# Kernel optimization log

Measured on AMD Instinct MI355X. Metric: run time of the kernel, lower is better.

Reference implementation:

```python
import jax, jax.numpy as jnp
import numpy as np

N_NODES = 100000
N_EDGES = 1600000
IN_DIM = 128
HID = 128
OUT_DIM = 64
N_LAYERS = 3


def setup_inputs() -> dict:
    key = jax.random.key(0)
    ks = jax.random.split(key, 8)
    x = jax.random.normal(ks[0], (N_NODES, IN_DIM), dtype=jnp.float32)
    edge_index = jax.random.randint(ks[1], (2, N_EDGES), 0, N_NODES, dtype=jnp.int64)
    s = 1.0 / np.sqrt(HID)
    Wl = jax.random.normal(ks[2], (N_LAYERS, HID, HID), dtype=jnp.float32) * s
    Wr = jax.random.normal(ks[3], (N_LAYERS, HID, HID), dtype=jnp.float32) * s
    b = jnp.zeros((N_LAYERS, HID), dtype=jnp.float32)
    fc_w = jax.random.normal(ks[4], (N_LAYERS * HID, OUT_DIM), dtype=jnp.float32) * (1.0 / np.sqrt(N_LAYERS * HID))
    fc_b = jnp.zeros((OUT_DIM,), dtype=jnp.float32)
    return {"x": x, "edge_index": edge_index, "Wl": Wl, "Wr": Wr, "b": b, "fc_w": fc_w, "fc_b": fc_b}


def _sage_conv(x, src, dst, Wl, Wr, b, n_nodes):
    # PyG SAGEConv (aggr='mean'): out = lin_l(mean_{j->i} x_j) + lin_r(x_i)
    msg = x[src]                                             # [E, d] gather
    agg = jax.ops.segment_sum(msg, dst, num_segments=n_nodes)  # [N, d]
    deg = jax.ops.segment_sum(jnp.ones((src.shape[0],), x.dtype), dst, num_segments=n_nodes)
    mean = agg / jnp.maximum(deg, 1.0)[:, None]
    return mean @ Wl + x @ Wr + b


def reference(x, edge_index, Wl, Wr, b, fc_w, fc_b):
    src, dst = edge_index[0], edge_index[1]
    n = x.shape[0]
    h = x
    layer_out = []
    for i in range(N_LAYERS):  # small fixed layer count
        h = jax.nn.relu(_sage_conv(h, src, dst, Wl[i], Wr[i], b[i], n))
        layer_out.append(h)  # dropout p=0 -> identity
    hk = jnp.concatenate(layer_out, axis=-1)  # JK 'cat': [N, L*HID]
    return hk @ fc_w + fc_b
```

## Files before the change

kernel.cpp:

```cpp
#include <hip/hip_runtime.h>
#include <hip/hip_bf16.h>
#include <stdint.h>

#define N_NODES 100000
#define N_EDGES 1600000
#define HID 128
#define OUT_DIM 64
#define N_LAYERS 3
#define CAP 64
#define CAP_SHIFT 6
#define BIN_NODES 256
#define NBIN2 ((N_NODES + BIN_NODES - 1) / BIN_NODES)
#define BINCAP 8192
#define EPT 8

typedef __attribute__((ext_vector_type(8))) short short8;
typedef __attribute__((ext_vector_type(4))) float v4f;
typedef __attribute__((ext_vector_type(4))) unsigned short ushort4v;

__device__ __forceinline__ float bf2f(unsigned int lo16) {
    union { unsigned int i; float f; } v; v.i = lo16 << 16; return v.f;
}
__device__ __forceinline__ unsigned short f2bf(float f) {
    union { float f; unsigned int i; } v; v.f = f;
    unsigned int r = v.i + 0x7fffu + ((v.i >> 16) & 1u);
    return (unsigned short)(r >> 16);
}

__device__ __forceinline__ void stage16(const void* g, void* l) {
    __builtin_amdgcn_global_load_lds(
        (const __attribute__((address_space(1))) unsigned int*)g,
        (__attribute__((address_space(3))) unsigned int*)l, 16, 0, 0);
}

#define CONV_N (N_NODES * HID / 4)
__global__ void prologue(const int* __restrict__ raw, int* __restrict__ flag,
                         int* __restrict__ bin_cnt,
                         const float* __restrict__ x, unsigned short* __restrict__ xb,
                         const float* __restrict__ Wl, const float* __restrict__ Wr,
                         const float* __restrict__ fc_w,
                         unsigned short* __restrict__ WlT, unsigned short* __restrict__ WrT,
                         unsigned short* __restrict__ fcT,
                         unsigned short* b0, unsigned short* b1, unsigned short* b2) {
    int gidx = blockIdx.x * blockDim.x + threadIdx.x;
    if (blockIdx.x == 0 && threadIdx.x < 64) {
        int v = raw[2 * threadIdx.x + 1];
        unsigned long long b = __ballot(v != 0);
        if (threadIdx.x == 0) *flag = (b == 0ull) ? 1 : 0;
    }
    if (gidx < NBIN2) bin_cnt[gidx] = 0;
    if (blockIdx.x == 1 && threadIdx.x < 192) {
        int t = threadIdx.x;
        unsigned short* bufs[3] = {b0, b1, b2};
        uint32_t* p = (uint32_t*)bufs[t >> 6];
        p[(size_t)N_NODES * 64 + (t & 63)] = 0;
    }

    if (gidx < CONV_N) {
        float4 v = ((const float4*)x)[gidx];
        ushort4v o;
        o[0] = f2bf(v.x); o[1] = f2bf(v.y); o[2] = f2bf(v.z); o[3] = f2bf(v.w);
        ((ushort4v*)xb)[gidx] = o;
        return;
    }
    int idx = gidx - CONV_N;
    const int WELEMS = N_LAYERS * HID * HID;
    if (idx < WELEMS) {
        int l = idx / (HID * HID);
        int rem = idx - l * HID * HID;
        int k = rem / HID, nn2 = rem - k * HID;
        WlT[l * HID * HID + nn2 * HID + k] = f2bf(Wl[idx]);
        WrT[l * HID * HID + nn2 * HID + k] = f2bf(Wr[idx]);
    } else {
        int j = idx - WELEMS;
        if (j < N_LAYERS * HID * OUT_DIM) {
            int l = j / (HID * OUT_DIM);
            int rem = j - l * HID * OUT_DIM;
            int k = rem / OUT_DIM, o = rem - k * OUT_DIM;
            fcT[l * OUT_DIM * HID + o * HID + k] = f2bf(fc_w[(l * HID + k) * OUT_DIM + o]);
        }
    }
}

__global__ __launch_bounds__(256) void fill_p1(const int* __restrict__ raw,
                                               const int* __restrict__ flag,
                                               int* __restrict__ bin_cnt,
                                               unsigned int* __restrict__ bins) {
    __shared__ int h[NBIN2];
    __shared__ int basekeep[NBIN2];
    int tid = threadIdx.x;
    for (int b = tid; b < NBIN2; b += 256) h[b] = 0;
    __syncthreads();

    int e0 = blockIdx.x * (256 * EPT) + tid;
    int s[EPT], d[EPT];
    bool is64 = (*flag != 0);
#pragma unroll
    for (int k = 0; k < EPT; ++k) {
        int e = e0 + k * 256;
        if (e < N_EDGES) {
            if (is64) {
                const long long* r = (const long long*)raw;
                d[k] = (int)r[N_EDGES + e];
                s[k] = (int)r[e];
            } else {
                d[k] = raw[N_EDGES + e];
                s[k] = raw[e];
            }
        } else {
            d[k] = -1;
        }
    }
#pragma unroll
    for (int k = 0; k < EPT; ++k)
        if (d[k] >= 0) atomicAdd(&h[d[k] >> 8], 1);
    __syncthreads();
    for (int b = tid; b < NBIN2; b += 256) {
        int c = h[b];
        basekeep[b] = c ? atomicAdd(&bin_cnt[b], c) : 0;
        h[b] = 0;
    }
    __syncthreads();
#pragma unroll
    for (int k = 0; k < EPT; ++k) {
        if (d[k] >= 0) {
            int b = d[k] >> 8;
            int off = basekeep[b] + atomicAdd(&h[b], 1);
            if (off < BINCAP)
                bins[(size_t)b * BINCAP + off] =
                    ((unsigned int)s[k] << 8) | (unsigned int)(d[k] & 255);
        }
    }
}

__global__ __launch_bounds__(256) void fill_p2(const int* __restrict__ bin_cnt,
                                               const unsigned int* __restrict__ bins,
                                               int* __restrict__ ell,
                                               int* __restrict__ deg,
                                               float* __restrict__ inv_deg, int n) {
    __shared__ int tile[BIN_NODES * CAP];
    __shared__ int cnt[BIN_NODES];
    int b = blockIdx.x, tid = threadIdx.x;
    for (int i = tid; i < BIN_NODES; i += 256) cnt[i] = 0;
    __syncthreads();

    int m = bin_cnt[b];
    if (m > BINCAP) m = BINCAP;
    for (int i = tid; i < m; i += 256) {
        unsigned int e = bins[(size_t)b * BINCAP + i];
        int dl = (int)(e & 255u);
        int slot = atomicAdd(&cnt[dl], 1);
        if (slot < CAP) tile[(dl << CAP_SHIFT) + slot] = (int)(e >> 8);
    }
    __syncthreads();

    int node0 = b << 8;
    for (int i = tid; i < BIN_NODES; i += 256) {
        int node = node0 + i;
        if (node < n) {
            int dgf = cnt[i];
            int dg = dgf > CAP ? CAP : dgf;
            deg[node] = dg;
            inv_deg[node] = 1.0f / (float)(dg > 0 ? dg : 1);
            int r = (dg + 7) & ~7;
            for (int p = dg; p < r; ++p) tile[(i << CAP_SHIFT) + p] = N_NODES;
        }
    }
    __syncthreads();

    const uint4* t4 = (const uint4*)tile;
    uint4* g4 = (uint4*)ell;
    for (int v = tid; v < BIN_NODES * 16; v += 256) {
        int row = v >> 4;
        int node = node0 + row;
        if (node < n) g4[((size_t)node << 4) + (v & 15)] = t4[v];
    }
}

__global__ __launch_bounds__(256) void agg_bf(
    const unsigned short* __restrict__ h, const int* __restrict__ ell,
    const int* __restrict__ deg, const float* __restrict__ inv_deg,
    unsigned short* __restrict__ meanb) {
    int tid = threadIdx.x;
    int grp = tid >> 4;
    int lane16 = tid & 15;
    int node = blockIdx.x * 16 + grp;
    bool valid = node < N_NODES;
    int nd = valid ? node : 0;
    int dg = valid ? deg[nd] : 0;
    int dgp = (dg + 7) & ~7;
    int base = nd << CAP_SHIFT;
    const uint4* hv = (const uint4*)h;
    float a[8];
#pragma unroll
    for (int c = 0; c < 8; ++c) a[c] = 0.f;

    for (int t = 0; t < dgp; t += 8) {
        int idx[8];
#pragma unroll
        for (int u = 0; u < 8; ++u) idx[u] = ell[base + t + u];
        uint4 v[8];
#pragma unroll
        for (int u = 0; u < 8; ++u) v[u] = hv[(size_t)idx[u] * 16 + lane16];
#pragma unroll
        for (int u = 0; u < 8; ++u) {
            a[0] += bf2f(v[u].x & 0xffffu); a[1] += bf2f(v[u].x >> 16);
            a[2] += bf2f(v[u].y & 0xffffu); a[3] += bf2f(v[u].y >> 16);
            a[4] += bf2f(v[u].z & 0xffffu); a[5] += bf2f(v[u].z >> 16);
            a[6] += bf2f(v[u].w & 0xffffu); a[7] += bf2f(v[u].w >> 16);
        }
    }
    if (valid) {
        float id = inv_deg[nd];
        uint4 o;
        o.x = (uint32_t)f2bf(a[0] * id) | ((uint32_t)f2bf(a[1] * id) << 16);
        o.y = (uint32_t)f2bf(a[2] * id) | ((uint32_t)f2bf(a[3] * id) << 16);
        o.z = (uint32_t)f2bf(a[4] * id) | ((uint32_t)f2bf(a[5] * id) << 16);
        o.w = (uint32_t)f2bf(a[6] * id) | ((uint32_t)f2bf(a[7] * id) << 16);
        *(uint4*)&meanb[(size_t)node * HID + lane16 * 8] = o;
    }
}

__global__ __launch_bounds__(256, 2) void layer_mfma(
    const unsigned short* __restrict__ Am,
    const unsigned short* __restrict__ Ah,
    const unsigned short* __restrict__ WlT,
    const unsigned short* __restrict__ WrT,
    const float* __restrict__ bias,
    unsigned short* __restrict__ Hout, int n) {
    __shared__ uint4 smA[128 * 16];
    __shared__ uint4 smB[128 * 16];
    int tid = threadIdx.x;
    int w = tid >> 6, L = tid & 63;
    int q = L >> 4, r16 = L & 15;
    int colbase = (w & 1) * 64;
    int nodebase = (w >> 1) * 64;
    int node0 = blockIdx.x * 128;

    {
        const unsigned short* srcs[2] = {Am, Ah};
#pragma unroll
        for (int op = 0; op < 2; ++op) {
            const unsigned short* S = srcs[op];
            char* D = (char*)(op ? smB : smA);
#pragma unroll
            for (int i = 0; i < 8; ++i) {
                int c = (w << 3) + i;
                int row_l = (c << 2) + (L >> 4);
                int chunk = (L & 15) ^ (row_l & 7);
                const unsigned short* src =
                    S + (((size_t)(node0 + row_l)) << 7) + (chunk << 3);
                stage16(src, D + (c << 10));
            }
        }
    }

    short8 wfr[2][4][4];
#pragma unroll
    for (int seg = 0; seg < 2; ++seg) {
        const unsigned short* WT = seg ? WrT : WlT;
#pragma unroll
        for (int t = 0; t < 4; ++t)
#pragma unroll
            for (int i = 0; i < 4; ++i)
                wfr[seg][t][i] =
                    *(const short8*)&WT[(colbase + i * 16 + r16) * HID + t * 32 + q * 8];
    }

    __syncthreads();

    v4f acc[4][4];
#pragma unroll
    for (int i = 0; i < 4; ++i)
#pragma unroll
        for (int j = 0; j < 4; ++j)
#pragma unroll
            for (int r = 0; r < 4; ++r) acc[i][j][r] = 0.f;

#pragma unroll
    for (int seg = 0; seg < 2; ++seg) {
        const uint4* SM = seg ? smB : smA;
#pragma unroll
        for (int t = 0; t < 4; ++t) {
            short8 bfr[4];
#pragma unroll
            for (int j = 0; j < 4; ++j) {
                int row = nodebase + j * 16 + r16;
                bfr[j] = *(const short8*)&SM[(row << 4) + ((t * 4 + q) ^ (row & 7))];
            }
#pragma unroll
            for (int i = 0; i < 4; ++i)
#pragma unroll
                for (int j = 0; j < 4; ++j)
                    acc[i][j] = __builtin_amdgcn_mfma_f32_16x16x32_bf16(
                        wfr[seg][t][i], bfr[j], acc[i][j], 0, 0, 0);
        }
    }

#pragma unroll
    for (int i = 0; i < 4; ++i) {
        int col = colbase + i * 16 + q * 4;
        float4 bv = *(const float4*)&bias[col];
#pragma unroll
        for (int j = 0; j < 4; ++j) {
            int node = node0 + nodebase + j * 16 + r16;
            if (node < n) {
                float v0 = acc[i][j][0] + bv.x;
                float v1 = acc[i][j][1] + bv.y;
                float v2 = acc[i][j][2] + bv.z;
                float v3 = acc[i][j][3] + bv.w;
                ushort4v o;
                o[0] = f2bf(v0 > 0.f ? v0 : 0.f);
                o[1] = f2bf(v1 > 0.f ? v1 : 0.f);
                o[2] = f2bf(v2 > 0.f ? v2 : 0.f);
                o[3] = f2bf(v3 > 0.f ? v3 : 0.f);
                *(ushort4v*)&Hout[(size_t)node * HID + col] = o;
            }
        }
    }
}

__global__ __launch_bounds__(256, 2) void layer3_fc(
    const unsigned short* __restrict__ Am,
    const unsigned short* __restrict__ Ah,
    const unsigned short* __restrict__ WlT,
    const unsigned short* __restrict__ WrT,
    const float* __restrict__ bias,
    const unsigned short* __restrict__ hA,
    const unsigned short* __restrict__ fcT,
    const float* __restrict__ fc_b,
    float* __restrict__ out, int n) {
    __shared__ uint4 smA[128 * 16];
    __shared__ uint4 smB[128 * 16];
    int tid = threadIdx.x;
    int w = tid >> 6, L = tid & 63;
    int q = L >> 4, r16 = L & 15;
    int colbase = (w & 1) * 64;
    int nodebase = (w >> 1) * 64;
    int node0 = blockIdx.x * 128;

    {
        const unsigned short* srcs[2] = {Am, Ah};
#pragma unroll
        for (int op = 0; op < 2; ++op) {
            const unsigned short* S = srcs[op];
            char* D = (char*)(op ? smB : smA);
#pragma unroll
            for (int i = 0; i < 8; ++i) {
                int c = (w << 3) + i;
                int row_l = (c << 2) + (L >> 4);
                int chunk = (L & 15) ^ (row_l & 7);
                const unsigned short* src =
                    S + (((size_t)(node0 + row_l)) << 7) + (chunk << 3);
                stage16(src, D + (c << 10));
            }
        }
    }

    short8 wfr[2][4][4];
#pragma unroll
    for (int seg = 0; seg < 2; ++seg) {
        const unsigned short* WT = seg ? WrT : WlT;
#pragma unroll
        for (int t = 0; t < 4; ++t)
#pragma unroll
            for (int i = 0; i < 4; ++i)
                wfr[seg][t][i] =
                    *(const short8*)&WT[(colbase + i * 16 + r16) * HID + t * 32 + q * 8];
    }

    __syncthreads();

    v4f acc[4][4];
#pragma unroll
    for (int i = 0; i < 4; ++i)
#pragma unroll
        for (int j = 0; j < 4; ++j)
#pragma unroll
            for (int r = 0; r < 4; ++r) acc[i][j][r] = 0.f;

#pragma unroll
    for (int seg = 0; seg < 2; ++seg) {
        const uint4* SM = seg ? smB : smA;
#pragma unroll
        for (int t = 0; t < 4; ++t) {
            short8 bfr[4];
#pragma unroll
            for (int j = 0; j < 4; ++j) {
                int row = nodebase + j * 16 + r16;
                bfr[j] = *(const short8*)&SM[(row << 4) + ((t * 4 + q) ^ (row & 7))];
            }
#pragma unroll
            for (int i = 0; i < 4; ++i)
#pragma unroll
                for (int j = 0; j < 4; ++j)
                    acc[i][j] = __builtin_amdgcn_mfma_f32_16x16x32_bf16(
                        wfr[seg][t][i], bfr[j], acc[i][j], 0, 0, 0);
        }
    }

    int nd2[2], gvalid[2];
#pragma unroll
    for (int j = 0; j < 2; ++j) {
        int t = node0 + w * 32 + j * 16 + r16;
        gvalid[j] = t < n;
        nd2[j] = gvalid[j] ? t : n - 1;
    }
    short8 ha[2][4];
#pragma unroll
    for (int j = 0; j < 2; ++j)
#pragma unroll
        for (int t = 0; t < 4; ++t)
            ha[j][t] = *(const short8*)&hA[(size_t)nd2[j] * HID + t * 32 + q * 8];

    __syncthreads();

#pragma unroll
    for (int i = 0; i < 4; ++i) {
        int col = colbase + i * 16 + q * 4;
        float4 bv = *(const float4*)&bias[col];
#pragma unroll
        for (int j = 0; j < 4; ++j) {
            int row = nodebase + j * 16 + r16;
            float v0 = acc[i][j][0] + bv.x;
            float v1 = acc[i][j][1] + bv.y;
            float v2 = acc[i][j][2] + bv.z;
            float v3 = acc[i][j][3] + bv.w;
            uint2 val;
            val.x = (uint32_t)f2bf(v0 > 0.f ? v0 : 0.f) |
                    ((uint32_t)f2bf(v1 > 0.f ? v1 : 0.f) << 16);
            val.y = (uint32_t)f2bf(v2 > 0.f ? v2 : 0.f) |
                    ((uint32_t)f2bf(v3 > 0.f ? v3 : 0.f) << 16);
            int slot = (col >> 3) ^ (row & 7);
            uint2* p2 = (uint2*)&smA[(row << 4) + slot];
            p2[q & 1] = val;
        }
    }
    __syncthreads();

    v4f acc2[4][2];
#pragma unroll
    for (int i = 0; i < 4; ++i) {
        float4 bv = *(const float4*)&fc_b[i * 16 + q * 4];
#pragma unroll
        for (int j = 0; j < 2; ++j) {
            acc2[i][j][0] = bv.x; acc2[i][j][1] = bv.y;
            acc2[i][j][2] = bv.z; acc2[i][j][3] = bv.w;
        }
    }

#pragma unroll
    for (int l = 0; l < 3; ++l) {
        const unsigned short* F = fcT + (size_t)l * OUT_DIM * HID;
#pragma unroll
        for (int t = 0; t < 4; ++t) {
            int koff = t * 32 + q * 8;
            short8 afr[4], bfr[2];
#pragma unroll
            for (int i = 0; i < 4; ++i)
                afr[i] = *(const short8*)&F[(i * 16 + r16) * HID + koff];
#pragma unroll
            for (int j = 0; j < 2; ++j) {
                int row = w * 32 + j * 16 + r16;
                if (l == 0)
                    bfr[j] = ha[j][t];
                else if (l == 1)
                    bfr[j] = *(const short8*)&smB[(row << 4) + ((t * 4 + q) ^ (row & 7))];
                else
                    bfr[j] = *(const short8*)&smA[(row << 4) + ((t * 4 + q) ^ (row & 7))];
            }
#pragma unroll
            for (int i = 0; i < 4; ++i)
#pragma unroll
                for (int j = 0; j < 2; ++j)
                    acc2[i][j] = __builtin_amdgcn_mfma_f32_16x16x32_bf16(afr[i], bfr[j], acc2[i][j], 0, 0, 0);
        }
    }

#pragma unroll
    for (int i = 0; i < 4; ++i)
#pragma unroll
        for (int j = 0; j < 2; ++j)
            if (gvalid[j])
                *(v4f*)&out[(size_t)nd2[j] * OUT_DIM + i * 16 + q * 4] = acc2[i][j];
}

extern "C" void kernel_launch(void* const* d_in, const int* in_sizes, int n_in,
                              void* d_out, int out_size, void* d_ws, size_t ws_size,
                              hipStream_t stream) {
    const float* x     = (const float*)d_in[0];
    const int*   edges = (const int*)d_in[1];
    const float* Wl    = (const float*)d_in[2];
    const float* Wr    = (const float*)d_in[3];
    const float* b     = (const float*)d_in[4];
    const float* fc_w  = (const float*)d_in[5];
    const float* fc_b  = (const float*)d_in[6];
    float* out = (float*)d_out;

    char* ws = (char*)d_ws;
    size_t off = 0;
    auto alloc = [&](size_t bytes) {
        void* p = ws + off;
        off = (off + bytes + 255) & ~(size_t)255;
        return p;
    };
    int*   flag    = (int*)alloc(256);
    int*   bin_cnt = (int*)alloc((size_t)NBIN2 * 4);
    int*   deg     = (int*)alloc((size_t)N_NODES * 4);
    float* inv_deg = (float*)alloc((size_t)N_NODES * 4);
    int*   ell     = (int*)alloc(((size_t)N_NODES * CAP + 64) * 4);
    unsigned int* bins = (unsigned int*)alloc((size_t)NBIN2 * BINCAP * 4);
    unsigned short* xb    = (unsigned short*)alloc((size_t)(N_NODES + 128) * HID * 2);
    unsigned short* meanb = (unsigned short*)alloc((size_t)(N_NODES + 128) * HID * 2);
    unsigned short* hA    = (unsigned short*)alloc((size_t)(N_NODES + 128) * HID * 2);
    unsigned short* hB    = (unsigned short*)alloc((size_t)(N_NODES + 128) * HID * 2);
    unsigned short* WlT   = (unsigned short*)alloc((size_t)N_LAYERS * HID * HID * 2);
    unsigned short* WrT   = (unsigned short*)alloc((size_t)N_LAYERS * HID * HID * 2);
    unsigned short* fcT   = (unsigned short*)alloc((size_t)N_LAYERS * OUT_DIM * HID * 2);

    const int PREP_TOTAL = CONV_N + N_LAYERS * HID * HID + N_LAYERS * HID * OUT_DIM;
    prologue<<<(PREP_TOTAL + 255) / 256, 256, 0, stream>>>(
        edges, flag, bin_cnt, x, xb, Wl, Wr, fc_w, WlT, WrT, fcT, xb, hA, hB);
    fill_p1<<<(N_EDGES + 256 * EPT - 1) / (256 * EPT), 256, 0, stream>>>(
        edges, flag, bin_cnt, bins);
    fill_p2<<<NBIN2, 256, 0, stream>>>(bin_cnt, bins, ell, deg, inv_deg, N_NODES);

    int ngrid = (N_NODES + 127) / 128;
    int agrid = (N_NODES + 15) / 16;

    agg_bf<<<agrid, 256, 0, stream>>>(xb, ell, deg, inv_deg, meanb);
    layer_mfma<<<ngrid, 256, 0, stream>>>(
        meanb, xb, WlT, WrT, b, hA, N_NODES);

    agg_bf<<<agrid, 256, 0, stream>>>(hA, ell, deg, inv_deg, meanb);
    layer_mfma<<<ngrid, 256, 0, stream>>>(
        meanb, hA, WlT + (size_t)HID * HID, WrT + (size_t)HID * HID, b + HID, hB, N_NODES);

    agg_bf<<<agrid, 256, 0, stream>>>(hB, ell, deg, inv_deg, meanb);
    layer3_fc<<<ngrid, 256, 0, stream>>>(
        meanb, hB, WlT + (size_t)2 * HID * HID, WrT + (size_t)2 * HID * HID, b + 2 * HID,
        hA, fcT, fc_b, out, N_NODES);
}
```

Measured before the change: 438.9 us.

## Merge prologue with edge binning and software-pipeline neighbor gathers

```diff
diff --git a/kernel.cpp b/kernel.cpp
--- a/kernel.cpp
+++ b/kernel.cpp
@@ -13,6 +13,7 @@
 #define NBIN2 ((N_NODES + BIN_NODES - 1) / BIN_NODES)
 #define BINCAP 8192
 #define EPT 8
+#define P1_BLOCKS ((N_EDGES + 256 * EPT - 1) / (256 * EPT))
 
 typedef __attribute__((ext_vector_type(8))) short short8;
 typedef __attribute__((ext_vector_type(4))) float v4f;
@@ -34,101 +35,99 @@
 }
 
 #define CONV_N (N_NODES * HID / 4)
-__global__ void prologue(const int* __restrict__ raw, int* __restrict__ flag,
-                         int* __restrict__ bin_cnt,
-                         const float* __restrict__ x, unsigned short* __restrict__ xb,
-                         const float* __restrict__ Wl, const float* __restrict__ Wr,
-                         const float* __restrict__ fc_w,
-                         unsigned short* __restrict__ WlT, unsigned short* __restrict__ WrT,
-                         unsigned short* __restrict__ fcT,
-                         unsigned short* b0, unsigned short* b1, unsigned short* b2) {
-    int gidx = blockIdx.x * blockDim.x + threadIdx.x;
-    if (blockIdx.x == 0 && threadIdx.x < 64) {
-        int v = raw[2 * threadIdx.x + 1];
-        unsigned long long b = __ballot(v != 0);
-        if (threadIdx.x == 0) *flag = (b == 0ull) ? 1 : 0;
-    }
-    if (gidx < NBIN2) bin_cnt[gidx] = 0;
-    if (blockIdx.x == 1 && threadIdx.x < 192) {
-        int t = threadIdx.x;
+__global__ __launch_bounds__(256) void merged_pre(
+    const int* __restrict__ raw,
+    int* __restrict__ bin_cnt, unsigned int* __restrict__ bins,
+    const float* __restrict__ x, unsigned short* __restrict__ xb,
+    const float* __restrict__ Wl, const float* __restrict__ Wr,
+    const float* __restrict__ fc_w,
+    unsigned short* __restrict__ WlT, unsigned short* __restrict__ WrT,
+    unsigned short* __restrict__ fcT,
+    unsigned short* b0, unsigned short* b1, unsigned short* b2) {
+    __shared__ int h[NBIN2];
+    __shared__ int basekeep[NBIN2];
+    __shared__ int sflag;
+    int blk = blockIdx.x, tid = threadIdx.x;
+
+    if (blk < P1_BLOCKS) {
+        if (tid < 64) {
+            int v = raw[2 * tid + 1];
+            unsigned long long bl = __ballot(v != 0);
+            if (tid == 0) sflag = (bl == 0ull) ? 1 : 0;
+        }
+        for (int b = tid; b < NBIN2; b += 256) h[b] = 0;
+        __syncthreads();
+        bool is64 = (sflag != 0);
+
+        int e0 = blk * (256 * EPT) + tid;
+        int s[EPT], d[EPT];
+#pragma unroll
+        for (int k = 0; k < EPT; ++k) {
+            int e = e0 + k * 256;
+            if (e < N_EDGES) {
+                if (is64) {
+                    const long long* r = (const long long*)raw;
+                    d[k] = (int)r[N_EDGES + e];
+                    s[k] = (int)r[e];
+                } else {
+                    d[k] = raw[N_EDGES + e];
+                    s[k] = raw[e];
+                }
+            } else {
+                d[k] = -1;
+            }
+        }
+#pragma unroll
+        for (int k = 0; k < EPT; ++k)
+            if (d[k] >= 0) atomicAdd(&h[d[k] >> 8], 1);
+        __syncthreads();
+        for (int b = tid; b < NBIN2; b += 256) {
+            int c = h[b];
+            basekeep[b] = c ? atomicAdd(&bin_cnt[b], c) : 0;
+            h[b] = 0;
+        }
+        __syncthreads();
+#pragma unroll
+        for (int k = 0; k < EPT; ++k) {
+            if (d[k] >= 0) {
+                int b = d[k] >> 8;
+                int off = basekeep[b] + atomicAdd(&h[b], 1);
+                if (off < BINCAP)
+                    bins[(size_t)b * BINCAP + off] =
+                        ((unsigned int)s[k] << 8) | (unsigned int)(d[k] & 255);
+            }
+        }
+    }
+
+    if (blk == P1_BLOCKS && tid < 192) {
         unsigned short* bufs[3] = {b0, b1, b2};
-        uint32_t* p = (uint32_t*)bufs[t >> 6];
-        p[(size_t)N_NODES * 64 + (t & 63)] = 0;
-    }
-
+        uint32_t* p = (uint32_t*)bufs[tid >> 6];
+        p[(size_t)N_NODES * 64 + (tid & 63)] = 0;
+    }
+
+    int gidx = blk * 256 + tid;
     if (gidx < CONV_N) {
         float4 v = ((const float4*)x)[gidx];
         ushort4v o;
         o[0] = f2bf(v.x); o[1] = f2bf(v.y); o[2] = f2bf(v.z); o[3] = f2bf(v.w);
         ((ushort4v*)xb)[gidx] = o;
-        return;
-    }
-    int idx = gidx - CONV_N;
-    const int WELEMS = N_LAYERS * HID * HID;
-    if (idx < WELEMS) {
-        int l = idx / (HID * HID);
-        int rem = idx - l * HID * HID;
-        int k = rem / HID, nn2 = rem - k * HID;
-        WlT[l * HID * HID + nn2 * HID + k] = f2bf(Wl[idx]);
-        WrT[l * HID * HID + nn2 * HID + k] = f2bf(Wr[idx]);
     } else {
-        int j = idx - WELEMS;
-        if (j < N_LAYERS * HID * OUT_DIM) {
-            int l = j / (HID * OUT_DIM);
-            int rem = j - l * HID * OUT_DIM;
-            int k = rem / OUT_DIM, o = rem - k * OUT_DIM;
-            fcT[l * OUT_DIM * HID + o * HID + k] = f2bf(fc_w[(l * HID + k) * OUT_DIM + o]);
-        }
-    }
-}
-
-__global__ __launch_bounds__(256) void fill_p1(const int* __restrict__ raw,
-                                               const int* __restrict__ flag,
-                                               int* __restrict__ bin_cnt,
-                                               unsigned int* __restrict__ bins) {
-    __shared__ int h[NBIN2];
-    __shared__ int basekeep[NBIN2];
-    int tid = threadIdx.x;
-    for (int b = tid; b < NBIN2; b += 256) h[b] = 0;
-    __syncthreads();
-
-    int e0 = blockIdx.x * (256 * EPT) + tid;
-    int s[EPT], d[EPT];
-    bool is64 = (*flag != 0);
-#pragma unroll
-    for (int k = 0; k < EPT; ++k) {
-        int e = e0 + k * 256;
-        if (e < N_EDGES) {
-            if (is64) {
-                const long long* r = (const long long*)raw;
-                d[k] = (int)r[N_EDGES + e];
-                s[k] = (int)r[e];
-            } else {
-                d[k] = raw[N_EDGES + e];
-                s[k] = raw[e];
-            }
+        int idx = gidx - CONV_N;
+        const int WELEMS = N_LAYERS * HID * HID;
+        if (idx < WELEMS) {
+            int l = idx / (HID * HID);
+            int rem = idx - l * HID * HID;
+            int k = rem / HID, nn2 = rem - k * HID;
+            WlT[l * HID * HID + nn2 * HID + k] = f2bf(Wl[idx]);
+            WrT[l * HID * HID + nn2 * HID + k] = f2bf(Wr[idx]);
         } else {
-            d[k] = -1;
-        }
-    }
-#pragma unroll
-    for (int k = 0; k < EPT; ++k)
-        if (d[k] >= 0) atomicAdd(&h[d[k] >> 8], 1);
-    __syncthreads();
-    for (int b = tid; b < NBIN2; b += 256) {
-        int c = h[b];
-        basekeep[b] = c ? atomicAdd(&bin_cnt[b], c) : 0;
-        h[b] = 0;
-    }
-    __syncthreads();
-#pragma unroll
-    for (int k = 0; k < EPT; ++k) {
-        if (d[k] >= 0) {
-            int b = d[k] >> 8;
-            int off = basekeep[b] + atomicAdd(&h[b], 1);
-            if (off < BINCAP)
-                bins[(size_t)b * BINCAP + off] =
-                    ((unsigned int)s[k] << 8) | (unsigned int)(d[k] & 255);
+            int j = idx - WELEMS;
+            if (j < N_LAYERS * HID * OUT_DIM) {
+                int l = j / (HID * OUT_DIM);
+                int rem = j - l * HID * OUT_DIM;
+                int k = rem / OUT_DIM, o = rem - k * OUT_DIM;
+                fcT[l * OUT_DIM * HID + o * HID + k] = f2bf(fc_w[(l * HID + k) * OUT_DIM + o]);
+            }
         }
     }
 }
@@ -174,6 +173,27 @@
         int row = v >> 4;
         int node = node0 + row;
         if (node < n) g4[((size_t)node << 4) + (v & 15)] = t4[v];
+    }
+}
+
+__device__ __forceinline__ void gather8(const uint4* __restrict__ hv,
+                                        int4 i0, int4 i1, int lane16, uint4 v[8]) {
+    v[0] = hv[(size_t)i0.x * 16 + lane16];
+    v[1] = hv[(size_t)i0.y * 16 + lane16];
+    v[2] = hv[(size_t)i0.z * 16 + lane16];
+    v[3] = hv[(size_t)i0.w * 16 + lane16];
+    v[4] = hv[(size_t)i1.x * 16 + lane16];
+    v[5] = hv[(size_t)i1.y * 16 + lane16];
+    v[6] = hv[(size_t)i1.z * 16 + lane16];
+    v[7] = hv[(size_t)i1.w * 16 + lane16];
+}
+__device__ __forceinline__ void accum8(const uint4 v[8], float a[8]) {
+#pragma unroll
+    for (int u = 0; u < 8; ++u) {
+        a[0] += bf2f(v[u].x & 0xffffu); a[1] += bf2f(v[u].x >> 16);
+        a[2] += bf2f(v[u].y & 0xffffu); a[3] += bf2f(v[u].y >> 16);
+        a[4] += bf2f(v[u].z & 0xffffu); a[5] += bf2f(v[u].z >> 16);
+        a[6] += bf2f(v[u].w & 0xffffu); a[7] += bf2f(v[u].w >> 16);
     }
 }
 
@@ -195,20 +215,27 @@
 #pragma unroll
     for (int c = 0; c < 8; ++c) a[c] = 0.f;
 
-    for (int t = 0; t < dgp; t += 8) {
-        int idx[8];
-#pragma unroll
-        for (int u = 0; u < 8; ++u) idx[u] = ell[base + t + u];
-        uint4 v[8];
-#pragma unroll
-        for (int u = 0; u < 8; ++u) v[u] = hv[(size_t)idx[u] * 16 + lane16];
-#pragma unroll
-        for (int u = 0; u < 8; ++u) {
-            a[0] += bf2f(v[u].x & 0xffffu); a[1] += bf2f(v[u].x >> 16);
-            a[2] += bf2f(v[u].y & 0xffffu); a[3] += bf2f(v[u].y >> 16);
-            a[4] += bf2f(v[u].z & 0xffffu); a[5] += bf2f(v[u].z >> 16);
-            a[6] += bf2f(v[u].w & 0xffffu); a[7] += bf2f(v[u].w >> 16);
-        }
+    if (dgp) {
+        uint4 vA[8], vB[8];
+        int4 i0 = *(const int4*)&ell[base + 0];
+        int4 i1 = *(const int4*)&ell[base + 4];
+        gather8(hv, i0, i1, lane16, vA);
+        int t = 8;
+        bool done = false;
+        while (t < dgp) {
+            i0 = *(const int4*)&ell[base + t];
+            i1 = *(const int4*)&ell[base + t + 4];
+            gather8(hv, i0, i1, lane16, vB);
+            accum8(vA, a);
+            t += 8;
+            if (t >= dgp) { accum8(vB, a); done = true; break; }
+            i0 = *(const int4*)&ell[base + t];
+            i1 = *(const int4*)&ell[base + t + 4];
+            gather8(hv, i0, i1, lane16, vA);
+            accum8(vB, a);
+            t += 8;
+        }
+        if (!done) accum8(vA, a);
     }
     if (valid) {
         float id = inv_deg[nd];
@@ -504,7 +531,6 @@
         off = (off + bytes + 255) & ~(size_t)255;
         return p;
     };
-    int*   flag    = (int*)alloc(256);
     int*   bin_cnt = (int*)alloc((size_t)NBIN2 * 4);
     int*   deg     = (int*)alloc((size_t)N_NODES * 4);
     float* inv_deg = (float*)alloc((size_t)N_NODES * 4);
@@ -518,11 +544,12 @@
     unsigned short* WrT   = (unsigned short*)alloc((size_t)N_LAYERS * HID * HID * 2);
     unsigned short* fcT   = (unsigned short*)alloc((size_t)N_LAYERS * OUT_DIM * HID * 2);
 
+    hipMemsetAsync(bin_cnt, 0, (size_t)NBIN2 * 4, stream);
+
     const int PREP_TOTAL = CONV_N + N_LAYERS * HID * HID + N_LAYERS * HID * OUT_DIM;
-    prologue<<<(PREP_TOTAL + 255) / 256, 256, 0, stream>>>(
-        edges, flag, bin_cnt, x, xb, Wl, Wr, fc_w, WlT, WrT, fcT, xb, hA, hB);
-    fill_p1<<<(N_EDGES + 256 * EPT - 1) / (256 * EPT), 256, 0, stream>>>(
-        edges, flag, bin_cnt, bins);
+    int pregrid = (PREP_TOTAL + 255) / 256;
+    merged_pre<<<pregrid, 256, 0, stream>>>(
+        edges, bin_cnt, bins, x, xb, Wl, Wr, fc_w, WlT, WrT, fcT, xb, hA, hB);
     fill_p2<<<NBIN2, 256, 0, stream>>>(bin_cnt, bins, ell, deg, inv_deg, N_NODES);
 
     int ngrid = (N_NODES + 127) / 128;
```

New measurement: 446.6 us. No clear change (+1.8%).
